# Kernel optimization log

Hardware: AMD Instinct MI355X
Metric: run time of the kernel (lower is better)

Reference implementation:

```python
import jax, jax.numpy as jnp
import numpy as np

B, N, IN, OUT, H = 8, 256, 256, 256, 4
HD = OUT // H  # 64
ALPHA = 0.2    # LeakyReLU negative slope
EPS = 1e-5


def layernorm(x, g, b):
    m = x.mean(-1, keepdims=True)
    v = jnp.mean(jnp.square(x - m), axis=-1, keepdims=True)
    return (x - m) / jnp.sqrt(v + EPS) * g + b


def setup_inputs() -> dict:
    key = jax.random.key(0)
    ks = jax.random.split(key, 16)
    s = 0.05
    return {
        'h':    jax.random.normal(ks[0], (B, N, IN), jnp.float32),
        'adj':  jax.random.randint(ks[1], (B, N, N), 0, 2, jnp.int32),
        # per-head params (leading dim H)
        'W':    jax.random.normal(ks[2], (H, IN, HD), jnp.float32) * s,      # node proj (no bias)
        'We1':  jax.random.normal(ks[3], (H, 2 * IN, HD), jnp.float32) * s,  # edge_encoder lin
        'be1':  jnp.zeros((H, HD), jnp.float32),
        'Wa1':  jax.random.normal(ks[4], (H, 3 * HD, HD), jnp.float32) * s,  # attn mlp lin1
        'ba1':  jnp.zeros((H, HD), jnp.float32),
        'wa2':  jax.random.normal(ks[5], (H, HD), jnp.float32) * s,          # attn mlp lin2 -> scalar
        'ba2':  jnp.zeros((H,), jnp.float32),
        'ln_g': jnp.ones((H, HD), jnp.float32),   # per-head LayerNorm
        'ln_b': jnp.zeros((H, HD), jnp.float32),
        'Wo':   jax.random.normal(ks[6], (OUT, OUT), jnp.float32) * s,       # output projection
        'bo':   jnp.zeros((OUT,), jnp.float32),
        'ln2_g': jnp.ones((OUT,), jnp.float32),   # final LayerNorm
        'ln2_b': jnp.zeros((OUT,), jnp.float32),
    }


def _head(h, adj_mask, W, We1, be1, Wa1, ba1, wa2, ba2, g, b):
    # h: [B,N,IN]; adj_mask: [B,N,N] bool (True where adj==0)
    Wh = jnp.einsum('bnf,fd->bnd', h, W)                      # [B,N,HD]
    # attention MLP lin1 applied to concat([Wh_i, Wh_j, edge]):
    # split weight so the per-node parts are computed once, broadcast over pairs
    Wa, Wb, We = Wa1[:HD], Wa1[HD:2 * HD], Wa1[2 * HD:]
    si = jnp.einsum('bnd,de->bne', Wh, Wa) + ba1              # [B,N,HD]
    sj = jnp.einsum('bnd,de->bne', Wh, Wb)                    # [B,N,HD]
    # edge encoder: Linear(cat[h_i,h_j]) -> leaky_relu, split likewise
    ei = jnp.einsum('bnf,fd->bnd', h, We1[:IN]) + be1         # [B,N,HD]
    ej = jnp.einsum('bnf,fd->bnd', h, We1[IN:])               # [B,N,HD]
    edge = jax.nn.leaky_relu(ei[:, :, None, :] + ej[:, None, :, :], ALPHA)  # [B,N,N,HD]
    hidden = jax.nn.leaky_relu(
        si[:, :, None, :] + sj[:, None, :, :] + jnp.einsum('bijd,de->bije', edge, We),
        ALPHA)                                                # [B,N,N,HD]
    e = jnp.einsum('bijd,d->bij', hidden, wa2) + ba2          # [B,N,N]
    e = jnp.where(adj_mask, -1e9, e)
    attn = jax.nn.softmax(e, axis=-1)                         # [B,N,N]
    hp = jnp.einsum('bij,bjd->bid', attn, Wh)                 # [B,N,HD]
    return layernorm(hp, g, b)


def reference(h, adj, W, We1, be1, Wa1, ba1, wa2, ba2, ln_g, ln_b, Wo, bo, ln2_g, ln2_b):
    adj_mask = (adj == 0)
    heads = [
        _head(h, adj_mask, W[i], We1[i], be1[i], Wa1[i], ba1[i],
              wa2[i], ba2[i], ln_g[i], ln_b[i])
        for i in range(H)
    ]
    concat = jnp.concatenate(heads, axis=-1)                  # [B,N,OUT]
    out = jnp.einsum('bnf,fo->bno', concat, Wo) + bo
    out = out + h                                             # residual (IN == OUT)
    return layernorm(out, ln2_g, ln2_b)
```

## Files before the change

### kernel.cpp

```cpp
#include <hip/hip_runtime.h>
#include <hip/hip_bf16.h>

#define B_ 8
#define N_ 256
#define IN_ 256
#define OUT_ 256
#define H_ 4
#define HD_ 64
#define ALPHA_ 0.2f
#define EPS_ 1e-5f

#define S_ (B_*H_*N_*HD_)


typedef unsigned short ushort_t;
typedef __attribute__((ext_vector_type(8))) short short8;
typedef __attribute__((ext_vector_type(4))) float floatx4;

__device__ __forceinline__ float lrelu(float x) { return fmaxf(x, ALPHA_ * x); }
__device__ __forceinline__ ushort_t f2b(float x) {
    unsigned u = __float_as_uint(x);
    unsigned r = ((u >> 16) & 1u) + 0x7fffu;
    return (ushort_t)((u + r) >> 16);
}
__device__ __forceinline__ unsigned pk2(float x0, float x1) {
    __hip_bfloat162 p = __float22bfloat162_rn(make_float2(x0, x1));
    return *(unsigned*)&p;
}

__global__ __launch_bounds__(256) void build_kernel(
    const float* __restrict__ h, const float* __restrict__ W,
    const float* __restrict__ We1, const float* __restrict__ Wa1,
    const float* __restrict__ Wo,
    ushort_t* __restrict__ h_b, ushort_t* __restrict__ wfull,
    ushort_t* __restrict__ wo_t, ushort_t* __restrict__ bw_b)
{
    const int blk = blockIdx.x;
    const int tid = threadIdx.x;
    const int r4 = tid >> 6, cl = tid & 63;

    if (blk < 512) {
        const int i = (blk * 256 + tid) * 4;
        float4 v = *(const float4*)&h[i];
        uint2 o; o.x = pk2(v.x, v.y); o.y = pk2(v.z, v.w);
        *(uint2*)&h_b[i] = o;
    } else if (blk < 560) {
        const int bb = blk - 512;
        const int hh = bb / 12, rem = bb % 12;
        const int cq = rem >> 2, ft = rem & 3;
        const int f0 = ft * 64;
        __shared__ float tl[64][65];
        for (int r = r4; r < 64; r += 4) {
            float v;
            if (cq == 0)      v = W  [((size_t)hh * 256 + f0 + r) * 64 + cl];
            else if (cq == 1) v = We1[((size_t)hh * 512 + f0 + r) * 64 + cl];
            else              v = We1[((size_t)hh * 512 + 256 + f0 + r) * 64 + cl];
            tl[r][cl] = v;
        }
        __syncthreads();
        for (int cr = r4; cr < 64; cr += 4)
            wfull[((size_t)hh * 256 + cq * 64 + cr) * 256 + f0 + cl] = f2b(tl[cl][cr]);
    } else if (blk < 576) {
        const int mm = blk - 560;
        const int hh = mm >> 2, ft = mm & 3;
        const int f0 = ft * 64;
        __shared__ float wlds[64][65];
        __shared__ float wa_l[64][65];
        __shared__ float tl[64][65];
        for (int r = r4; r < 64; r += 4) {
            wlds[r][cl] = W[((size_t)hh * 256 + f0 + r) * 64 + cl];
            wa_l[r][cl] = Wa1[((size_t)hh * 192 + r) * 64 + cl];
        }
        __syncthreads();
        for (int f = r4; f < 64; f += 4) {
            float acc = 0.f;
            #pragma unroll 8
            for (int g = 0; g < 64; ++g) acc += wlds[f][g] * wa_l[g][cl];
            tl[f][cl] = acc;
        }
        __syncthreads();
        for (int cr = r4; cr < 64; cr += 4)
            wfull[((size_t)hh * 256 + 192 + cr) * 256 + f0 + cl] = f2b(tl[cl][cr]);
    } else if (blk < 592) {
        const int bb = blk - 576;
        const int to = bb & 3, tf = bb >> 2;
        __shared__ float t[64][65];
        for (int rr = r4; rr < 64; rr += 4)
            t[rr][cl] = Wo[(size_t)(tf * 64 + rr) * 256 + to * 64 + cl];
        __syncthreads();
        for (int rr = r4; rr < 64; rr += 4)
            wo_t[(size_t)(to * 64 + rr) * 256 + tf * 64 + cl] = f2b(t[cl][rr]);
    } else {
        const int hh = blk - 592;
        for (int idx = tid; idx < 64 * 128; idx += 256) {
            const int e = idx >> 7, k = idx & 127;
            const int row = (k < 64) ? (128 + k) : k;
            bw_b[hh * 8192 + idx] = f2b(Wa1[(size_t)hh * 192 * 64 + row * 64 + e]);
        }
    }
}

__global__ __launch_bounds__(256) void prep2_kernel(
    const ushort_t* __restrict__ h_b, const ushort_t* __restrict__ wfull,
    const float* __restrict__ be1, const float* __restrict__ ba1,
    float* __restrict__ ws)
{
    const int gm = blockIdx.x & 127, gn = blockIdx.x >> 7;
    const int tid = threadIdx.x, lane = tid & 63, wid = tid >> 6;
    const int quad = lane >> 4, l15 = lane & 15;

    float*    ei_f = ws;
    float*    si_f = ws + S_;
    ushort_t* ej_b = (ushort_t*)(ws + 2 * (size_t)S_);
    ushort_t* Wh_b = ej_b + S_;
    ushort_t* WhT_b = (ushort_t*)(ws + 4 * (size_t)S_) + 262144 + 65536 + 32768;

    floatx4 acc[2];
    #pragma unroll
    for (int nt = 0; nt < 2; ++nt) acc[nt] = (floatx4){0.f,0.f,0.f,0.f};

    #pragma unroll 2
    for (int ks = 0; ks < 8; ++ks) {
        short8 afr = *(const short8*)&h_b[(size_t)(gm * 16 + l15) * 256 + ks * 32 + quad * 8];
        #pragma unroll
        for (int nt = 0; nt < 2; ++nt) {
            short8 bfr = *(const short8*)&wfull[(size_t)(gn * 128 + wid * 32 + nt * 16 + l15) * 256 + ks * 32 + quad * 8];
            acc[nt] = __builtin_amdgcn_mfma_f32_16x16x32_bf16(afr, bfr, acc[nt], 0, 0, 0);
        }
    }

    #pragma unroll
    for (int nt = 0; nt < 2; ++nt) {
        const int colg = gn * 128 + wid * 32 + nt * 16 + l15;
        const int head = colg >> 8, c = colg & 255, type = c >> 6, d = c & 63;
        #pragma unroll
        for (int reg = 0; reg < 4; ++reg) {
            const int row = gm * 16 + quad * 4 + reg;
            const int b = row >> 8, n = row & 255;
            const size_t idx = ((size_t)(b * H_ + head) * 256 + n) * 64 + d;
            const float v = acc[nt][reg];
            if (type == 0) {
                const ushort_t vb = f2b(v);
                Wh_b[idx] = vb;
                WhT_b[((size_t)(b * H_ + head) * 64 + d) * 256 + n] = vb;
            }
            else if (type == 1) ei_f[idx] = v + be1[head * 64 + d];
            else if (type == 2) ej_b[idx] = f2b(v);
            else                si_f[idx] = v + ba1[head * 64 + d];
        }
    }
}

__global__ __launch_bounds__(256, 2) void attn_kernel(
    const int* __restrict__ adj, const float* __restrict__ wa2,
    const float* __restrict__ ba2, const float* __restrict__ ln_g,
    const float* __restrict__ ln_b, float* __restrict__ ws)
{
    const int blk  = blockIdx.x;
    const int ig   = blk & 15;
    const int head = (blk >> 4) & 3;
    const int b    = blk >> 6;
    const int i0   = ig * 16;
    const int tid  = threadIdx.x;
    const int lane = tid & 63;
    const int wid  = tid >> 6;
    const int quad = lane >> 4;
    const int l15  = lane & 15;
    const int bh   = b * H_ + head;

    __shared__ float    P_s[16 * 256];
    __shared__ ushort_t Pb_s[16 * 264];
    __shared__ float    ei_s[16 * 64];
    __shared__ float    si_s[16 * 64];
    __shared__ unsigned long long adjm_s[16 * 4];
    __shared__ float    hp_s[16 * 68];

    const float*    ei_f = ws;
    const float*    si_f = ws + S_;
    const ushort_t* ej_b = (const ushort_t*)(ws + 2 * (size_t)S_);
    const ushort_t* Wh_b = ej_b + S_;
    ushort_t*       conc = (ushort_t*)(ws + 3 * (size_t)S_) + 524288;
    const ushort_t* bw_b = (const ushort_t*)(ws + 4 * (size_t)S_) + 262144 + 65536;
    const ushort_t* WhT_b = bw_b + 32768;

    {
        const int ii = tid >> 4, c = tid & 15;
        *(float4*)&ei_s[ii * 64 + c * 4] =
            *(const float4*)&ei_f[((size_t)(bh * 256 + i0 + ii)) * 64 + c * 4];
        *(float4*)&si_s[ii * 64 + c * 4] =
            *(const float4*)&si_f[((size_t)(bh * 256 + i0 + ii)) * 64 + c * 4];
    }
    {
        int av[16];
        #pragma unroll
        for (int r = 0; r < 16; ++r)
            av[r] = adj[((size_t)(b * 256 + i0 + r)) * 256 + tid];
        #pragma unroll
        for (int r = 0; r < 16; ++r) {
            unsigned long long mk = __ballot(av[r] != 0);
            if (lane == 0) adjm_s[r * 4 + wid] = mk;
        }
    }

    uint4   ejr[4][2];
    short8  afrWe[4][2];
    floatx4 sjaccT[4][4];
    float   w6[4][4], w4[4][4];
    #pragma unroll
    for (int nt = 0; nt < 4; ++nt) {
        const size_t jrow = (size_t)(bh * 256 + wid * 64 + nt * 16 + l15) * 64;
        #pragma unroll
        for (int kk = 0; kk < 2; ++kk)
            ejr[nt][kk] = *(const uint4*)&ej_b[jrow + kk * 32 + quad * 8];
    }
    #pragma unroll
    for (int mt = 0; mt < 4; ++mt) {
        #pragma unroll
        for (int ks = 0; ks < 2; ++ks)
            afrWe[mt][ks] = *(const short8*)&bw_b[head * 8192 + (mt * 16 + l15) * 128 + ks * 32 + quad * 8];
        float4 wvv = *(const float4*)&wa2[head * 64 + mt * 16 + quad * 4];
        w6[mt][0] = 0.6f * wvv.x; w4[mt][0] = 0.4f * wvv.x;
        w6[mt][1] = 0.6f * wvv.y; w4[mt][1] = 0.4f * wvv.y;
        w6[mt][2] = 0.6f * wvv.z; w4[mt][2] = 0.4f * wvv.z;
        w6[mt][3] = 0.6f * wvv.w; w4[mt][3] = 0.4f * wvv.w;
    }
    {
        #pragma unroll
        for (int mt = 0; mt < 4; ++mt)
            #pragma unroll
            for (int nt = 0; nt < 4; ++nt) sjaccT[mt][nt] = (floatx4){0.f,0.f,0.f,0.f};
        #pragma unroll
        for (int ks = 2; ks < 4; ++ks) {
            short8 aWb[4], bWh[4];
            #pragma unroll
            for (int mt = 0; mt < 4; ++mt)
                aWb[mt] = *(const short8*)&bw_b[head * 8192 + (mt * 16 + l15) * 128 + ks * 32 + quad * 8];
            #pragma unroll
            for (int nt = 0; nt < 4; ++nt)
                bWh[nt] = *(const short8*)&Wh_b[((size_t)(bh * 256 + wid * 64 + nt * 16 + l15)) * 64
                                                + (ks - 2) * 32 + quad * 8];
            #pragma unroll
            for (int mt = 0; mt < 4; ++mt)
                #pragma unroll
                for (int nt = 0; nt < 4; ++nt)
                    sjaccT[mt][nt] = __builtin_amdgcn_mfma_f32_16x16x32_bf16(
                        aWb[mt], bWh[nt], sjaccT[mt][nt], 0, 0, 0);
        }
    }
    const float ba2h = ba2[head];

    __syncthreads();

    for (int i = 0; i < 16; ++i) {
        floatx4 acc[4][4];
        #pragma unroll
        for (int ks = 0; ks < 2; ++ks) {
            short8 tfr[4];
            float ev[8];
            *(float4*)&ev[0] = *(const float4*)&ei_s[i * 64 + ks * 32 + quad * 8];
            *(float4*)&ev[4] = *(const float4*)&ei_s[i * 64 + ks * 32 + quad * 8 + 4];
            #pragma unroll
            for (int nt = 0; nt < 4; ++nt) {
                const unsigned* rw = (const unsigned*)&ejr[nt][ks];
                union { unsigned u[4]; short8 s; } ow;
                #pragma unroll
                for (int p = 0; p < 4; ++p) {
                    float x0 = __uint_as_float(rw[p] << 16)         + ev[2 * p];
                    float x1 = __uint_as_float(rw[p] & 0xffff0000u) + ev[2 * p + 1];
                    ow.u[p] = pk2(lrelu(x0), lrelu(x1));
                }
                tfr[nt] = ow.s;
            }
            if (ks == 0) {
                #pragma unroll
                for (int mt = 0; mt < 4; ++mt)
                    #pragma unroll
                    for (int nt = 0; nt < 4; ++nt)
                        acc[mt][nt] = __builtin_amdgcn_mfma_f32_16x16x32_bf16(
                            afrWe[mt][0], tfr[nt], sjaccT[mt][nt], 0, 0, 0);
            } else {
                #pragma unroll
                for (int mt = 0; mt < 4; ++mt)
                    #pragma unroll
                    for (int nt = 0; nt < 4; ++nt)
                        acc[mt][nt] = __builtin_amdgcn_mfma_f32_16x16x32_bf16(
                            afrWe[mt][1], tfr[nt], acc[mt][nt], 0, 0, 0);
            }
        }

        float sv[4][4];
        #pragma unroll
        for (int mt = 0; mt < 4; ++mt)
            *(float4*)&sv[mt][0] = *(const float4*)&si_s[i * 64 + mt * 16 + quad * 4];
        #pragma unroll
        for (int nt = 0; nt < 4; ++nt) {
            float val = 0.f;
            #pragma unroll
            for (int mt = 0; mt < 4; ++mt)
                #pragma unroll
                for (int reg = 0; reg < 4; ++reg) {
                    const float t = acc[mt][nt][reg] + sv[mt][reg];
                    val = fmaf(t, w6[mt][reg], val);
                    val = fmaf(fabsf(t), w4[mt][reg], val);
                }
            val += __shfl_xor(val, 16, 64);
            val += __shfl_xor(val, 32, 64);
            if (quad == 0)
                P_s[i * 256 + wid * 64 + nt * 16 + l15] = val + ba2h;
        }
    }
    __syncthreads();

    #pragma unroll
    for (int rr = 0; rr < 4; ++rr) {
        const int r = rr * 4 + wid;
        float4 v = *(const float4*)&P_s[r * 256 + lane * 4];
        const unsigned mk = (unsigned)(adjm_s[r * 4 + quad] >> (l15 * 4)) & 0xFu;
        float v0 = (mk & 1u) ? v.x : -1e9f;
        float v1 = (mk & 2u) ? v.y : -1e9f;
        float v2 = (mk & 4u) ? v.z : -1e9f;
        float v3 = (mk & 8u) ? v.w : -1e9f;
        float m = fmaxf(fmaxf(v0, v1), fmaxf(v2, v3));
        #pragma unroll
        for (int off = 32; off >= 1; off >>= 1) m = fmaxf(m, __shfl_xor(m, off, 64));
        float p0 = __expf(v0 - m), p1 = __expf(v1 - m);
        float p2 = __expf(v2 - m), p3 = __expf(v3 - m);
        float s = (p0 + p1) + (p2 + p3);
        #pragma unroll
        for (int off = 32; off >= 1; off >>= 1) s += __shfl_xor(s, off, 64);
        const float inv = 1.f / s;
        uint2 o; o.x = pk2(p0 * inv, p1 * inv); o.y = pk2(p2 * inv, p3 * inv);
        *(uint2*)&Pb_s[r * 264 + lane * 4] = o;
    }
    __syncthreads();

    floatx4 hacc = (floatx4){0.f,0.f,0.f,0.f};
    #pragma unroll
    for (int s = 0; s < 8; ++s) {
        short8 af = *(const short8*)&Pb_s[l15 * 264 + s * 32 + quad * 8];
        short8 bf = *(const short8*)&WhT_b[((size_t)(bh * 64) + wid * 16 + l15) * 256 + s * 32 + quad * 8];
        hacc = __builtin_amdgcn_mfma_f32_16x16x32_bf16(af, bf, hacc, 0, 0, 0);
    }
    #pragma unroll
    for (int reg = 0; reg < 4; ++reg)
        hp_s[(quad * 4 + reg) * 68 + wid * 16 + l15] = hacc[reg];
    __syncthreads();

    const float gg = ln_g[head * 64 + lane];
    const float bb = ln_b[head * 64 + lane];
    #pragma unroll
    for (int pss = 0; pss < 4; ++pss) {
        const int r = pss * 4 + wid;
        const float v = hp_s[r * 68 + lane];
        float s1 = v, s2 = v * v;
        #pragma unroll
        for (int off = 32; off >= 1; off >>= 1) {
            s1 += __shfl_xor(s1, off, 64);
            s2 += __shfl_xor(s2, off, 64);
        }
        const float mean = s1 * (1.f / 64.f);
        const float var = s2 * (1.f / 64.f) - mean * mean;
        const float o = (v - mean) * __frsqrt_rn(var + EPS_) * gg + bb;
        conc[((size_t)(b * 256 + i0 + r)) * 256 + head * 64 + lane] = f2b(o);
    }
}

__global__ __launch_bounds__(256) void out2_kernel(
    const float* __restrict__ h, const float* __restrict__ bo,
    const float* __restrict__ ln2_g, const float* __restrict__ ln2_b,
    const ushort_t* __restrict__ conc, const ushort_t* __restrict__ wo_t,
    float* __restrict__ out)
{
    const int rowbase = blockIdx.x * 8;
    const int tid = threadIdx.x, lane = tid & 63, wid = tid >> 6;
    const int quad = lane >> 4, l15 = lane & 15;

    __shared__ float s1a[8][4], s2a[8][4];

    floatx4 acc[4];
    #pragma unroll
    for (int nt = 0; nt < 4; ++nt) acc[nt] = (floatx4){0.f,0.f,0.f,0.f};

    #pragma unroll 2
    for (int ks = 0; ks < 8; ++ks) {
        short8 afr = *(const short8*)&conc[(size_t)(rowbase + (l15 & 7)) * 256 + ks * 32 + quad * 8];
        #pragma unroll
        for (int nt = 0; nt < 4; ++nt) {
            short8 bfr = *(const short8*)&wo_t[(size_t)(wid * 64 + nt * 16 + l15) * 256 + ks * 32 + quad * 8];
            acc[nt] = __builtin_amdgcn_mfma_f32_16x16x32_bf16(afr, bfr, acc[nt], 0, 0, 0);
        }
    }

    float x[4][4];
    if (quad < 2) {
        float s1[4], s2[4];
        #pragma unroll
        for (int reg = 0; reg < 4; ++reg) { s1[reg] = 0.f; s2[reg] = 0.f; }
        #pragma unroll
        for (int nt = 0; nt < 4; ++nt) {
            const int col = wid * 64 + nt * 16 + l15;
            const float bv = bo[col];
            #pragma unroll
            for (int reg = 0; reg < 4; ++reg) {
                const int row = rowbase + quad * 4 + reg;
                float v = acc[nt][reg] + bv + h[(size_t)row * 256 + col];
                x[nt][reg] = v;
                s1[reg] += v;
                s2[reg] += v * v;
            }
        }
        #pragma unroll
        for (int reg = 0; reg < 4; ++reg) {
            #pragma unroll
            for (int off = 1; off <= 8; off <<= 1) {
                s1[reg] += __shfl_xor(s1[reg], off, 64);
                s2[reg] += __shfl_xor(s2[reg], off, 64);
            }
            if (l15 == 0) {
                s1a[quad * 4 + reg][wid] = s1[reg];
                s2a[quad * 4 + reg][wid] = s2[reg];
            }
        }
    }
    __syncthreads();

    if (quad < 2) {
        #pragma unroll
        for (int reg = 0; reg < 4; ++reg) {
            const int r = quad * 4 + reg;
            const float S1 = s1a[r][0] + s1a[r][1] + s1a[r][2] + s1a[r][3];
            const float S2 = s2a[r][0] + s2a[r][1] + s2a[r][2] + s2a[r][3];
            const float mean = S1 * (1.f / 256.f);
            const float var = S2 * (1.f / 256.f) - mean * mean;
            const float rs = __frsqrt_rn(var + EPS_);
            const int row = rowbase + r;
            #pragma unroll
            for (int nt = 0; nt < 4; ++nt) {
                const int col = wid * 64 + nt * 16 + l15;
                out[(size_t)row * 256 + col] =
                    (x[nt][reg] - mean) * rs * ln2_g[col] + ln2_b[col];
            }
        }
    }
}

extern "C" void kernel_launch(void* const* d_in, const int* in_sizes, int n_in,
                              void* d_out, int out_size, void* d_ws, size_t ws_size,
                              hipStream_t stream)
{
    const float* h    = (const float*)d_in[0];
    const int*   adj  = (const int*)  d_in[1];
    const float* W    = (const float*)d_in[2];
    const float* We1  = (const float*)d_in[3];
    const float* be1  = (const float*)d_in[4];
    const float* Wa1  = (const float*)d_in[5];
    const float* ba1  = (const float*)d_in[6];
    const float* wa2  = (const float*)d_in[7];
    const float* ba2  = (const float*)d_in[8];
    const float* ln_g = (const float*)d_in[9];
    const float* ln_b = (const float*)d_in[10];
    const float* Wo   = (const float*)d_in[11];
    const float* bo   = (const float*)d_in[12];
    const float* ln2g = (const float*)d_in[13];
    const float* ln2b = (const float*)d_in[14];

    float* ws = (float*)d_ws;
    ushort_t* h_b   = (ushort_t*)(ws + 3 * (size_t)S_);
    ushort_t* conc  = h_b + 524288;
    ushort_t* wfull = (ushort_t*)(ws + 4 * (size_t)S_);
    ushort_t* wo_t  = wfull + 262144;
    ushort_t* bw_b  = wo_t + 65536;
    float* out = (float*)d_out;

    build_kernel<<<596,  256, 0, stream>>>(h, W, We1, Wa1, Wo, h_b, wfull, wo_t, bw_b);
    prep2_kernel<<<1024, 256, 0, stream>>>(h_b, wfull, be1, ba1, ws);
    attn_kernel <<<512,  256, 0, stream>>>(adj, wa2, ba2, ln_g, ln_b, ws);
    out2_kernel <<<256,  256, 0, stream>>>(h, bo, ln2g, ln2b, conc, wo_t, out);
}
```

Measured before the change: 175.0 us.

## Fuse h bf16 conversion into projection GEMM and drop transposed Wh copy

The separate pass that converted h to bf16 in the build kernel is removed. The projection kernel now loads fp32 h directly and packs it to bf16 in registers before the MFMA. The transposed WhT buffer is no longer written; the attention kernel instead gathers the B fragment from row-major Wh_b with eight strided 16-bit loads per MFMA step. This saves a full round trip of h through memory and one scattered transposed store, but prep2 now reads twice the bytes for h and the attention GEMM's B loads become uncoalesced scalar gathers.

New measurement: 176.6 us. Within noise of the previous version (+0.9%).

```diff
diff --git a/kernel.cpp b/kernel.cpp
--- a/kernel.cpp
+++ b/kernel.cpp
@@ -29,24 +29,17 @@
 }
 
 __global__ __launch_bounds__(256) void build_kernel(
-    const float* __restrict__ h, const float* __restrict__ W,
-    const float* __restrict__ We1, const float* __restrict__ Wa1,
-    const float* __restrict__ Wo,
-    ushort_t* __restrict__ h_b, ushort_t* __restrict__ wfull,
-    ushort_t* __restrict__ wo_t, ushort_t* __restrict__ bw_b)
+    const float* __restrict__ W, const float* __restrict__ We1,
+    const float* __restrict__ Wa1, const float* __restrict__ Wo,
+    ushort_t* __restrict__ wfull, ushort_t* __restrict__ wo_t,
+    ushort_t* __restrict__ bw_b)
 {
     const int blk = blockIdx.x;
     const int tid = threadIdx.x;
     const int r4 = tid >> 6, cl = tid & 63;
 
-    if (blk < 512) {
-        const int i = (blk * 256 + tid) * 4;
-        float4 v = *(const float4*)&h[i];
-        uint2 o; o.x = pk2(v.x, v.y); o.y = pk2(v.z, v.w);
-        *(uint2*)&h_b[i] = o;
-    } else if (blk < 560) {
-        const int bb = blk - 512;
-        const int hh = bb / 12, rem = bb % 12;
+    if (blk < 48) {
+        const int hh = blk / 12, rem = blk % 12;
         const int cq = rem >> 2, ft = rem & 3;
         const int f0 = ft * 64;
         __shared__ float tl[64][65];
@@ -60,8 +53,8 @@
         __syncthreads();
         for (int cr = r4; cr < 64; cr += 4)
             wfull[((size_t)hh * 256 + cq * 64 + cr) * 256 + f0 + cl] = f2b(tl[cl][cr]);
-    } else if (blk < 576) {
-        const int mm = blk - 560;
+    } else if (blk < 64) {
+        const int mm = blk - 48;
         const int hh = mm >> 2, ft = mm & 3;
         const int f0 = ft * 64;
         __shared__ float wlds[64][65];
@@ -81,8 +74,8 @@
         __syncthreads();
         for (int cr = r4; cr < 64; cr += 4)
             wfull[((size_t)hh * 256 + 192 + cr) * 256 + f0 + cl] = f2b(tl[cl][cr]);
-    } else if (blk < 592) {
-        const int bb = blk - 576;
+    } else if (blk < 80) {
+        const int bb = blk - 64;
         const int to = bb & 3, tf = bb >> 2;
         __shared__ float t[64][65];
         for (int rr = r4; rr < 64; rr += 4)
@@ -91,7 +84,7 @@
         for (int rr = r4; rr < 64; rr += 4)
             wo_t[(size_t)(to * 64 + rr) * 256 + tf * 64 + cl] = f2b(t[cl][rr]);
     } else {
-        const int hh = blk - 592;
+        const int hh = blk - 80;
         for (int idx = tid; idx < 64 * 128; idx += 256) {
             const int e = idx >> 7, k = idx & 127;
             const int row = (k < 64) ? (128 + k) : k;
@@ -101,7 +94,7 @@
 }
 
 __global__ __launch_bounds__(256) void prep2_kernel(
-    const ushort_t* __restrict__ h_b, const ushort_t* __restrict__ wfull,
+    const float* __restrict__ h, const ushort_t* __restrict__ wfull,
     const float* __restrict__ be1, const float* __restrict__ ba1,
     float* __restrict__ ws)
 {
@@ -113,7 +106,6 @@
     float*    si_f = ws + S_;
     ushort_t* ej_b = (ushort_t*)(ws + 2 * (size_t)S_);
     ushort_t* Wh_b = ej_b + S_;
-    ushort_t* WhT_b = (ushort_t*)(ws + 4 * (size_t)S_) + 262144 + 65536 + 32768;
 
     floatx4 acc[2];
     #pragma unroll
@@ -121,11 +113,16 @@
 
     #pragma unroll 2
     for (int ks = 0; ks < 8; ++ks) {
-        short8 afr = *(const short8*)&h_b[(size_t)(gm * 16 + l15) * 256 + ks * 32 + quad * 8];
+        const float* hp0 = &h[(size_t)(gm * 16 + l15) * 256 + ks * 32 + quad * 8];
+        float4 a0 = *(const float4*)hp0;
+        float4 a1 = *(const float4*)(hp0 + 4);
+        union { unsigned u[4]; short8 s; } aw;
+        aw.u[0] = pk2(a0.x, a0.y); aw.u[1] = pk2(a0.z, a0.w);
+        aw.u[2] = pk2(a1.x, a1.y); aw.u[3] = pk2(a1.z, a1.w);
         #pragma unroll
         for (int nt = 0; nt < 2; ++nt) {
             short8 bfr = *(const short8*)&wfull[(size_t)(gn * 128 + wid * 32 + nt * 16 + l15) * 256 + ks * 32 + quad * 8];
-            acc[nt] = __builtin_amdgcn_mfma_f32_16x16x32_bf16(afr, bfr, acc[nt], 0, 0, 0);
+            acc[nt] = __builtin_amdgcn_mfma_f32_16x16x32_bf16(aw.s, bfr, acc[nt], 0, 0, 0);
         }
     }
 
@@ -139,11 +136,7 @@
             const int b = row >> 8, n = row & 255;
             const size_t idx = ((size_t)(b * H_ + head) * 256 + n) * 64 + d;
             const float v = acc[nt][reg];
-            if (type == 0) {
-                const ushort_t vb = f2b(v);
-                Wh_b[idx] = vb;
-                WhT_b[((size_t)(b * H_ + head) * 64 + d) * 256 + n] = vb;
-            }
+            if      (type == 0) Wh_b[idx] = f2b(v);
             else if (type == 1) ei_f[idx] = v + be1[head * 64 + d];
             else if (type == 2) ej_b[idx] = f2b(v);
             else                si_f[idx] = v + ba1[head * 64 + d];
@@ -181,7 +174,6 @@
     const ushort_t* Wh_b = ej_b + S_;
     ushort_t*       conc = (ushort_t*)(ws + 3 * (size_t)S_) + 524288;
     const ushort_t* bw_b = (const ushort_t*)(ws + 4 * (size_t)S_) + 262144 + 65536;
-    const ushort_t* WhT_b = bw_b + 32768;
 
     {
         const int ii = tid >> 4, c = tid & 15;
@@ -338,7 +330,10 @@
     #pragma unroll
     for (int s = 0; s < 8; ++s) {
         short8 af = *(const short8*)&Pb_s[l15 * 264 + s * 32 + quad * 8];
-        short8 bf = *(const short8*)&WhT_b[((size_t)(bh * 64) + wid * 16 + l15) * 256 + s * 32 + quad * 8];
+        short8 bf;
+        #pragma unroll
+        for (int jj = 0; jj < 8; ++jj)
+            bf[jj] = (short)Wh_b[((size_t)(bh * 256) + s * 32 + quad * 8 + jj) * 64 + wid * 16 + l15];
         hacc = __builtin_amdgcn_mfma_f32_16x16x32_bf16(af, bf, hacc, 0, 0, 0);
     }
     #pragma unroll
@@ -465,15 +460,14 @@
     const float* ln2b = (const float*)d_in[14];
 
     float* ws = (float*)d_ws;
-    ushort_t* h_b   = (ushort_t*)(ws + 3 * (size_t)S_);
-    ushort_t* conc  = h_b + 524288;
+    ushort_t* conc  = (ushort_t*)(ws + 3 * (size_t)S_) + 524288;
     ushort_t* wfull = (ushort_t*)(ws + 4 * (size_t)S_);
     ushort_t* wo_t  = wfull + 262144;
     ushort_t* bw_b  = wo_t + 65536;
     float* out = (float*)d_out;
 
-    build_kernel<<<596,  256, 0, stream>>>(h, W, We1, Wa1, Wo, h_b, wfull, wo_t, bw_b);
-    prep2_kernel<<<1024, 256, 0, stream>>>(h_b, wfull, be1, ba1, ws);
+    build_kernel<<<84,   256, 0, stream>>>(W, We1, Wa1, Wo, wfull, wo_t, bw_b);
+    prep2_kernel<<<1024, 256, 0, stream>>>(h, wfull, be1, ba1, ws);
     attn_kernel <<<512,  256, 0, stream>>>(adj, wa2, ba2, ln_g, ln_b, ws);
     out2_kernel <<<256,  256, 0, stream>>>(h, bo, ln2g, ln2b, conc, wo_t, out);
 }
```
